# Kernel optimization log

Measured on AMD Instinct MI355X. Metric: run time of the kernel, lower is better.

## Reference

```python
import jax, jax.numpy as jnp
import numpy as np

B, N, H = 32, 1024, 128
EPS = 1e-5


def setup_inputs() -> dict:
    key = jax.random.key(0)
    ks = jax.random.split(key, 9)
    node_embeddings = jax.random.normal(ks[0], (B, N, H), dtype=jnp.float32)
    edge_relations = jax.random.normal(ks[1], (B, N, N, 3), dtype=jnp.float32)
    adjacency = jax.random.randint(ks[2], (N, N), 0, 2, dtype=jnp.int32)
    s_msg = 1.0 / np.sqrt(H + 3)
    s_upd = 1.0 / np.sqrt(2 * H)
    W_msg = jax.random.uniform(ks[3], (H, H + 3), jnp.float32, -s_msg, s_msg)
    b_msg = jax.random.uniform(ks[4], (H,), jnp.float32, -s_msg, s_msg)
    W_upd = jax.random.uniform(ks[5], (H, 2 * H), jnp.float32, -s_upd, s_upd)
    b_upd = jax.random.uniform(ks[6], (H,), jnp.float32, -s_upd, s_upd)
    gamma = jnp.ones((H,), jnp.float32)
    beta = jnp.zeros((H,), jnp.float32)
    return {"node_embeddings": node_embeddings, "edge_relations": edge_relations,
            "adjacency": adjacency, "W_msg": W_msg, "b_msg": b_msg,
            "W_upd": W_upd, "b_upd": b_upd, "gamma": gamma, "beta": beta}


def reference(node_embeddings, edge_relations, adjacency, W_msg, b_msg, W_upd, b_upd, gamma, beta):
    # node_embeddings: [B,N,H]; edge_relations: [B,N,N,3]; adjacency: [N,N]
    b_, n_, h_ = node_embeddings.shape
    mask = (adjacency > 0).astype(node_embeddings.dtype)  # mask[j,i]=1 if i is neighbor of j
    # Split msg_nn weight: Linear(cat(h_i, e_ij)) = h_i @ W_h^T + e_ij @ W_e^T + b
    W_h = W_msg[:, :h_]   # [H,H]
    W_e = W_msg[:, h_:]   # [H,3]
    h_part = jnp.einsum('bih,oh->bio', node_embeddings, W_h)       # [B,N,H]
    msg_h = jnp.einsum('ji,bio->bjo', mask, h_part)                # aggregate sender linear part
    e_agg = jnp.einsum('bijc,ji->bjc', edge_relations, mask)       # aggregate edge feats first (memory-bound)
    msg_e = jnp.einsum('bjc,oc->bjo', e_agg, W_e)
    deg = mask.sum(axis=1)                                         # [N] in-degree of j
    messages = msg_h + msg_e + deg[None, :, None] * b_msg          # bias added once per edge
    # Dropout(0.2) is identity in inference; BatchNorm uses batch stats (training-mode math).
    upd_in = jnp.concatenate([node_embeddings, messages], axis=-1)  # [B,N,2H]
    updated = jax.nn.relu(jnp.einsum('bjk,ok->bjo', upd_in, W_upd) + b_upd)
    flat = updated.reshape(-1, h_)
    mean = flat.mean(axis=0)
    var = flat.var(axis=0)  # biased, as BatchNorm1d
    normed = (flat - mean) * jax.lax.rsqrt(var + EPS) * gamma + beta
    return normed.reshape(b_, n_, h_) + node_embeddings
```

## Files before the change

kernel.cpp:

```cpp
#include <hip/hip_runtime.h>

typedef _Float16 f16;
typedef f16 f16x4 __attribute__((ext_vector_type(4)));
typedef f16 f16x8 __attribute__((ext_vector_type(8)));
typedef float f32x4 __attribute__((ext_vector_type(4)));

#define BB 32
#define NN 1024
#define HH 128
#define ROWS (BB*NN)
#define EPS 1e-5f

__device__ __forceinline__ f16 f2h(float x) { return (f16)x; }

typedef __attribute__((address_space(1))) const void gv_t;
typedef __attribute__((address_space(3))) void lv_t;
__device__ __forceinline__ void gl_lds16(const void* g, void* l) {
  __builtin_amdgcn_global_load_lds((gv_t*)g, (lv_t*)l, 16, 0, 0);
}

__global__ __launch_bounds__(256) void prep0_k(
    const float* __restrict__ W_msg, const float* __restrict__ W_upd,
    const float* __restrict__ node, const int* __restrict__ adj,
    f16* __restrict__ Wh, f16* __restrict__ Wupd, float* __restrict__ We,
    float* __restrict__ e_agg, float* __restrict__ deg, float* __restrict__ sums,
    f16* __restrict__ nodeh, f16* __restrict__ maskf, f16* __restrict__ maskT)
{
  const int blk = blockIdx.x, t = threadIdx.x;
  if (blk == 0) {
    for (int idx = t; idx < HH*HH; idx += 256) {
      const int o = idx >> 7, h = idx & 127;
      Wh[idx] = f2h(W_msg[o*131 + h]);
    }
  } else if (blk == 1) {
    for (int idx = t; idx < HH*256; idx += 256)
      Wupd[idx] = f2h(W_upd[idx]);
  } else if (blk == 2) {
    for (int idx = t; idx < HH*3; idx += 256)
      We[idx] = W_msg[(idx/3)*131 + 128 + (idx % 3)];
    if (t < 256) sums[t] = 0.f;
  } else if (blk < 7) {
    const int base = (blk - 3) * 24576 + t;
    #pragma unroll
    for (int r = 0; r < 96; r++) e_agg[base + r*256] = 0.f;
  } else if (blk < 15) {
    __shared__ f16 ldsT[128][136];
    __shared__ float degl[128];
    const int tj = blk - 7;
    if (t < 128) degl[t] = 0.f;
    __syncthreads();
    for (int ti = 0; ti < 8; ti++) {
      #pragma unroll
      for (int pass = 0; pass < 16; pass++) {
        const int q = pass*256 + t;
        const int row = q >> 5, c4 = (q & 31) << 2;
        const int4 m = *(const int4*)&adj[(long)(tj*128 + row)*NN + ti*128 + c4];
        f16x4 hv;
        hv[0] = (m.x > 0) ? (f16)1.0f : (f16)0.0f;
        hv[1] = (m.y > 0) ? (f16)1.0f : (f16)0.0f;
        hv[2] = (m.z > 0) ? (f16)1.0f : (f16)0.0f;
        hv[3] = (m.w > 0) ? (f16)1.0f : (f16)0.0f;
        *(f16x4*)&maskf[(long)(tj*128 + row)*NN + ti*128 + c4] = hv;
        ldsT[c4 + 0][row] = hv[0];
        ldsT[c4 + 1][row] = hv[1];
        ldsT[c4 + 2][row] = hv[2];
        ldsT[c4 + 3][row] = hv[3];
        const int cnt = (m.x > 0) + (m.y > 0) + (m.z > 0) + (m.w > 0);
        if (cnt) atomicAdd(&degl[row], (float)cnt);
      }
      __syncthreads();
      #pragma unroll
      for (int pass = 0; pass < 8; pass++) {
        const int q = pass*256 + t;
        const int rT = q >> 4, c8 = (q & 15) << 3;
        *(uint4*)&maskT[(long)(ti*128 + rT)*NN + tj*128 + c8] =
            *(const uint4*)&ldsT[rT][c8];
      }
      __syncthreads();
    }
    if (t < 128) deg[tj*128 + t] = degl[t];
  } else {
    const long base = (long)(blk - 15)*256 + t;
    #pragma unroll
    for (int p = 0; p < 64; p++) {
      const long idx = base + (long)p*16384;
      const float4 v = ((const float4*)node)[idx];
      f16x4 hv; hv[0] = f2h(v.x); hv[1] = f2h(v.y); hv[2] = f2h(v.z); hv[3] = f2h(v.w);
      *(f16x4*)&nodeh[idx << 2] = hv;
    }
  }
}

__global__ __launch_bounds__(256) void phaseB_k(
    const f16* __restrict__ nodeh, const float* __restrict__ E,
    const f16* __restrict__ maskT, const f16* __restrict__ Wh,
    f16* __restrict__ h_part_T, float* __restrict__ e_agg)
{
  __shared__ f16 As[128*32];
  __shared__ f16 Bs[128*32];
  const int tid = threadIdx.x;

  if (blockIdx.x >= 256) {
    const int e  = blockIdx.x - 256;
    const int bb = e >> 5;
    const int r5 = e & 31;
    const int jt = r5 & 3;
    const int ih = r5 >> 2;
    const int j  = (jt << 8) + tid;
    const int i0 = ih << 7;
    const float* Ep = E + (long)bb*3145728 + (long)i0*3072 + (long)j*3;
    const f16*   Mp = maskT + (long)i0*NN + j;
    float a0 = 0.f, a1 = 0.f, a2 = 0.f;
    for (int ii = 0; ii < 128; ii += 8) {
      float m[8];
      #pragma unroll
      for (int v = 0; v < 8; v++) m[v] = (float)Mp[(long)(ii + v)*NN];
      float ev[8][3];
      #pragma unroll
      for (int v = 0; v < 8; v++) {
        const float* q = Ep + (long)(ii + v)*3072;
        ev[v][0] = q[0]; ev[v][1] = q[1]; ev[v][2] = q[2];
      }
      #pragma unroll
      for (int v = 0; v < 8; v++) {
        a0 = fmaf(m[v], ev[v][0], a0);
        a1 = fmaf(m[v], ev[v][1], a1);
        a2 = fmaf(m[v], ev[v][2], a2);
      }
    }
    const long eb = ((long)bb*NN + j)*3;
    atomicAdd(&e_agg[eb],     a0);
    atomicAdd(&e_agg[eb + 1], a1);
    atomicAdd(&e_agg[eb + 2], a2);
    return;
  }

  const int g  = blockIdx.x;
  const int nt = g & 7, bb = g >> 3;
  const int nbase = nt << 7;
  const int lane = tid & 63, wave = tid >> 6;
  const int wm = (wave & 1) << 6, wn = (wave >> 1) << 6;

  f32x4 acc[2][4], acc2[2][4];
  #pragma unroll
  for (int i = 0; i < 2; i++)
    #pragma unroll
    for (int j = 0; j < 4; j++)
      #pragma unroll
      for (int r = 0; r < 4; r++) { acc[i][j][r] = 0.f; acc2[i][j][r] = 0.f; }

  for (int k0 = 0; k0 < HH; k0 += 32) {
    #pragma unroll
    for (int p = 0; p < 2; p++) {
      const int q = (p << 8) + tid;
      const int row = q >> 2, kp = (q & 3) << 3;
      gl_lds16(&Wh[(long)row*HH + k0 + kp], &As[q << 3]);
      gl_lds16(&nodeh[(long)((bb << 10) + nbase + row)*HH + k0 + kp], &Bs[q << 3]);
    }
    __syncthreads();
    f16x8 af[4], bf[4];
    #pragma unroll
    for (int i = 0; i < 4; i++) {
      af[i] = *(const f16x8*)&As[((wm + (i << 4) + (lane & 15)) << 5) + ((lane >> 4) << 3)];
      bf[i] = *(const f16x8*)&Bs[((wn + (i << 4) + (lane & 15)) << 5) + ((lane >> 4) << 3)];
    }
    #pragma unroll
    for (int i = 0; i < 2; i++)
      #pragma unroll
      for (int j = 0; j < 4; j++) {
        acc[i][j]  = __builtin_amdgcn_mfma_f32_16x16x32_f16(af[i],     bf[j], acc[i][j],  0, 0, 0);
        acc2[i][j] = __builtin_amdgcn_mfma_f32_16x16x32_f16(af[i + 2], bf[j], acc2[i][j], 0, 0, 0);
      }
    __syncthreads();
  }

  f16* out = h_part_T + (long)bb * (HH*NN);
  const int rb = (lane >> 4) << 2, cb = lane & 15;
  #pragma unroll
  for (int i = 0; i < 4; i++)
    #pragma unroll
    for (int r = 0; r < 4; r++) {
      const int gm = wm + (i << 4) + rb + r;
      #pragma unroll
      for (int j = 0; j < 4; j++) {
        const int gn = nbase + wn + (j << 4) + cb;
        const float v = (i < 2) ? acc[i][j][r] : acc2[i - 2][j][r];
        out[(long)gm*NN + gn] = f2h(v);
      }
    }
}

__global__ __launch_bounds__(256) void gemm1_k(
    const f16* __restrict__ maskf, const f16* __restrict__ hp,
    const float* __restrict__ deg, const float* __restrict__ b_msg,
    const float* __restrict__ e_agg, const float* __restrict__ We,
    f16* __restrict__ msgs)
{
  const int mt = blockIdx.x, bb = blockIdx.z;
  const int jb = mt << 7;
  __shared__ f16 As[128*32];
  __shared__ f16 Bs[128*32];
  const int tid = threadIdx.x, lane = tid & 63, wave = tid >> 6;
  const int wm = (wave & 1) << 6, wn = (wave >> 1) << 6;

  f32x4 acc[4][4];
  #pragma unroll
  for (int i = 0; i < 4; i++)
    #pragma unroll
    for (int j = 0; j < 4; j++)
      #pragma unroll
      for (int r = 0; r < 4; r++) acc[i][j][r] = 0.f;

  for (int k0 = 0; k0 < NN; k0 += 32) {
    #pragma unroll
    for (int p = 0; p < 2; p++) {
      const int q = (p << 8) + tid;
      const int row = q >> 2, kp = (q & 3) << 3;
      gl_lds16(&maskf[(long)(jb + row)*NN + k0 + kp], &As[q << 3]);
      gl_lds16(&hp[(long)bb*(HH*NN) + (long)row*NN + k0 + kp], &Bs[q << 3]);
    }
    __syncthreads();
    f16x8 af[4], bf[4];
    #pragma unroll
    for (int i = 0; i < 4; i++) {
      af[i] = *(const f16x8*)&As[((wm + (i << 4) + (lane & 15)) << 5) + ((lane >> 4) << 3)];
      bf[i] = *(const f16x8*)&Bs[((wn + (i << 4) + (lane & 15)) << 5) + ((lane >> 4) << 3)];
    }
    #pragma unroll
    for (int i = 0; i < 4; i++)
      #pragma unroll
      for (int j = 0; j < 4; j++)
        acc[i][j] = __builtin_amdgcn_mfma_f32_16x16x32_f16(af[i], bf[j], acc[i][j], 0, 0, 0);
    __syncthreads();
  }

  const int rb = (lane >> 4) << 2, cb = lane & 15;
  #pragma unroll
  for (int i = 0; i < 4; i++)
    #pragma unroll
    for (int r = 0; r < 4; r++) {
      const int gm = jb + wm + (i << 4) + rb + r;
      const float dg = deg[gm];
      const long eb = ((long)bb*NN + gm)*3;
      const float e0 = e_agg[eb], e1 = e_agg[eb+1], e2 = e_agg[eb+2];
      #pragma unroll
      for (int j = 0; j < 4; j++) {
        const int gn = wn + (j << 4) + cb;
        const float v = acc[i][j][r] + dg*b_msg[gn]
                      + e0*We[gn*3] + e1*We[gn*3+1] + e2*We[gn*3+2];
        msgs[((long)bb*NN + gm)*HH + gn] = f2h(v);
      }
    }
}

__global__ __launch_bounds__(256) void gemm2_k(
    const f16* __restrict__ nodeh, const f16* __restrict__ msgs,
    const f16* __restrict__ Wupd, const float* __restrict__ b_upd,
    f16* __restrict__ upd, float* __restrict__ sums)
{
  const int mt = blockIdx.x;
  const int rowb = mt << 7;
  __shared__ f16 As[128*32];
  __shared__ f16 Bs[128*32];
  __shared__ float colS[128], colQ[128];
  const int tid = threadIdx.x, lane = tid & 63, wave = tid >> 6;
  const int wm = (wave & 1) << 6, wn = (wave >> 1) << 6;
  if (tid < 128) { colS[tid] = 0.f; colQ[tid] = 0.f; }

  f32x4 acc[4][4];
  #pragma unroll
  for (int i = 0; i < 4; i++)
    #pragma unroll
    for (int j = 0; j < 4; j++)
      #pragma unroll
      for (int r = 0; r < 4; r++) acc[i][j][r] = 0.f;

  for (int k0 = 0; k0 < 256; k0 += 32) {
    #pragma unroll
    for (int p = 0; p < 2; p++) {
      const int q = (p << 8) + tid;
      const int row = q >> 2, kp = (q & 3) << 3;
      const f16* src = (k0 < HH)
        ? &nodeh[(long)(rowb + row)*HH + k0 + kp]
        : &msgs[(long)(rowb + row)*HH + (k0 - HH) + kp];
      gl_lds16(src, &As[q << 3]);
      gl_lds16(&Wupd[(long)row*256 + k0 + kp], &Bs[q << 3]);
    }
    __syncthreads();
    f16x8 af[4], bf[4];
    #pragma unroll
    for (int i = 0; i < 4; i++) {
      af[i] = *(const f16x8*)&As[((wm + (i << 4) + (lane & 15)) << 5) + ((lane >> 4) << 3)];
      bf[i] = *(const f16x8*)&Bs[((wn + (i << 4) + (lane & 15)) << 5) + ((lane >> 4) << 3)];
    }
    #pragma unroll
    for (int i = 0; i < 4; i++)
      #pragma unroll
      for (int j = 0; j < 4; j++)
        acc[i][j] = __builtin_amdgcn_mfma_f32_16x16x32_f16(af[i], bf[j], acc[i][j], 0, 0, 0);
    __syncthreads();
  }

  const int rb = (lane >> 4) << 2, cb = lane & 15;
  float bup[4], s[4] = {0,0,0,0}, qq[4] = {0,0,0,0};
  #pragma unroll
  for (int j = 0; j < 4; j++) bup[j] = b_upd[wn + (j << 4) + cb];
  #pragma unroll
  for (int i = 0; i < 4; i++)
    #pragma unroll
    for (int r = 0; r < 4; r++) {
      const int gm = rowb + wm + (i << 4) + rb + r;
      #pragma unroll
      for (int j = 0; j < 4; j++) {
        const int gn = wn + (j << 4) + cb;
        const float v = fmaxf(acc[i][j][r] + bup[j], 0.f);
        upd[(long)gm*HH + gn] = f2h(v);
        s[j] += v; qq[j] += v*v;
      }
    }
  #pragma unroll
  for (int j = 0; j < 4; j++) {
    const int gn = wn + (j << 4) + cb;
    atomicAdd(&colS[gn], s[j]);
    atomicAdd(&colQ[gn], qq[j]);
  }
  __syncthreads();
  if (tid < 128) {
    atomicAdd(&sums[tid],       colS[tid]);
    atomicAdd(&sums[128 + tid], colQ[tid]);
  }
}

__global__ __launch_bounds__(256) void final_k(const f16* __restrict__ upd,
    const float* __restrict__ node, const float* __restrict__ sums,
    const float* __restrict__ gamma, const float* __restrict__ beta,
    float* __restrict__ out)
{
  const long idx = (long)blockIdx.x*256 + threadIdx.x;
  const f16x4 u  = *(const f16x4*)&upd[idx << 2];
  const float4 nd = ((const float4*)node)[idx];
  const int ob = (idx & 31) << 2;
  const float inv = 1.0f/32768.0f;
  float4 res;
  #pragma unroll
  for (int c = 0; c < 4; c++) {
    const float m  = sums[ob + c]*inv;
    const float va = sums[128 + ob + c]*inv - m*m;
    const float sc = rsqrtf(va + EPS)*gamma[ob + c];
    ((float*)&res)[c] = ((float)u[c] - m)*sc + beta[ob + c]
                      + ((const float*)&nd)[c];
  }
  ((float4*)out)[idx] = res;
}

extern "C" void kernel_launch(void* const* d_in, const int* in_sizes, int n_in,
                              void* d_out, int out_size, void* d_ws, size_t ws_size,
                              hipStream_t stream) {
  const float* node  = (const float*)d_in[0];
  const float* E     = (const float*)d_in[1];
  const int*   adj   = (const int*)  d_in[2];
  const float* W_msg = (const float*)d_in[3];
  const float* b_msg = (const float*)d_in[4];
  const float* W_upd = (const float*)d_in[5];
  const float* b_upd = (const float*)d_in[6];
  const float* gamma = (const float*)d_in[7];
  const float* beta  = (const float*)d_in[8];
  float* out = (float*)d_out;

  char* p = (char*)d_ws;
  auto alloc = [&](size_t n) { void* r = (void*)p; p += (n + 255) & ~(size_t)255; return r; };
  f16*   h_part_T = (f16*)  alloc((size_t)BB*HH*NN*2);
  f16*   msgs     = (f16*)  alloc((size_t)ROWS*HH*2);
  f16*   upd      = (f16*)  alloc((size_t)ROWS*HH*2);
  f16*   nodeh    = (f16*)  alloc((size_t)ROWS*HH*2);
  f16*   maskf    = (f16*)  alloc((size_t)NN*NN*2);
  f16*   maskT    = (f16*)  alloc((size_t)NN*NN*2);
  float* e_agg    = (float*)alloc((size_t)BB*NN*3*4);
  f16*   Wh       = (f16*)  alloc((size_t)HH*HH*2);
  f16*   Wupd     = (f16*)  alloc((size_t)HH*256*2);
  float* We       = (float*)alloc((size_t)HH*3*4);
  float* deg      = (float*)alloc((size_t)NN*4);
  float* sums     = (float*)alloc((size_t)256*4);

  prep0_k<<<79, 256, 0, stream>>>(W_msg, W_upd, node, adj,
                                  Wh, Wupd, We, e_agg, deg, sums,
                                  nodeh, maskf, maskT);

  phaseB_k<<<1280, 256, 0, stream>>>(nodeh, E, maskT, Wh, h_part_T, e_agg);

  gemm1_k<<<dim3(8, 1, BB), 256, 0, stream>>>(maskf, h_part_T, deg, b_msg, e_agg, We, msgs);

  gemm2_k<<<256, 256, 0, stream>>>(nodeh, msgs, Wupd, b_upd, upd, sums);

  final_k<<<4096, 256, 0, stream>>>(upd, node, sums, gamma, beta, out);
}
```

Before: 690.5 us.

## Stage edge reads through LDS, fold degree bias into h_part, re-split prep work

The edge-aggregation blocks now copy contiguous 8-row chunks of edge_relations into LDS with global_load_lds, so global reads are coalesced instead of stride-3 per thread. The mask fragments are still read from global memory. The degree-times-bias term is folded into h_part as an added b_msg before the mask GEMM, which removes the deg computation and its LDS atomics. Prep work is spread over 131 blocks with one tile per transpose block, and the e_agg and sums zeroing moves to hipMemsetAsync. This adds extra launches and syncs in exchange for better memory coalescing and balance.

```diff
diff --git a/kernel.cpp b/kernel.cpp
--- a/kernel.cpp
+++ b/kernel.cpp
@@ -23,84 +23,70 @@
     const float* __restrict__ W_msg, const float* __restrict__ W_upd,
     const float* __restrict__ node, const int* __restrict__ adj,
     f16* __restrict__ Wh, f16* __restrict__ Wupd, float* __restrict__ We,
-    float* __restrict__ e_agg, float* __restrict__ deg, float* __restrict__ sums,
     f16* __restrict__ nodeh, f16* __restrict__ maskf, f16* __restrict__ maskT)
 {
   const int blk = blockIdx.x, t = threadIdx.x;
-  if (blk == 0) {
+  if (blk < 64) {
+    const long base = (long)blk*16384 + t;
+    #pragma unroll
+    for (int p = 0; p < 64; p++) {
+      const long idx = base + (long)p*256;
+      const float4 v = ((const float4*)node)[idx];
+      f16x4 hv; hv[0] = f2h(v.x); hv[1] = f2h(v.y); hv[2] = f2h(v.z); hv[3] = f2h(v.w);
+      *(f16x4*)&nodeh[idx << 2] = hv;
+    }
+  } else if (blk < 128) {
+    __shared__ f16 ldsT[128][136];
+    const int tt = blk - 64, tj = tt >> 3, ti = tt & 7;
+    #pragma unroll
+    for (int p = 0; p < 16; p++) {
+      const int q = p*256 + t;
+      const int row = q >> 5, c4 = (q & 31) << 2;
+      const int4 m = *(const int4*)&adj[(long)(tj*128 + row)*NN + ti*128 + c4];
+      f16x4 hv;
+      hv[0] = (m.x > 0) ? (f16)1.0f : (f16)0.0f;
+      hv[1] = (m.y > 0) ? (f16)1.0f : (f16)0.0f;
+      hv[2] = (m.z > 0) ? (f16)1.0f : (f16)0.0f;
+      hv[3] = (m.w > 0) ? (f16)1.0f : (f16)0.0f;
+      *(f16x4*)&maskf[(long)(tj*128 + row)*NN + ti*128 + c4] = hv;
+      ldsT[c4 + 0][row] = hv[0];
+      ldsT[c4 + 1][row] = hv[1];
+      ldsT[c4 + 2][row] = hv[2];
+      ldsT[c4 + 3][row] = hv[3];
+    }
+    __syncthreads();
+    #pragma unroll
+    for (int p = 0; p < 8; p++) {
+      const int q = p*256 + t;
+      const int rT = q >> 4, c8 = (q & 15) << 3;
+      *(uint4*)&maskT[(long)(ti*128 + rT)*NN + tj*128 + c8] =
+          *(const uint4*)&ldsT[rT][c8];
+    }
+  } else if (blk == 128) {
     for (int idx = t; idx < HH*HH; idx += 256) {
       const int o = idx >> 7, h = idx & 127;
       Wh[idx] = f2h(W_msg[o*131 + h]);
     }
-  } else if (blk == 1) {
+  } else if (blk == 129) {
     for (int idx = t; idx < HH*256; idx += 256)
       Wupd[idx] = f2h(W_upd[idx]);
-  } else if (blk == 2) {
+  } else {
     for (int idx = t; idx < HH*3; idx += 256)
       We[idx] = W_msg[(idx/3)*131 + 128 + (idx % 3)];
-    if (t < 256) sums[t] = 0.f;
-  } else if (blk < 7) {
-    const int base = (blk - 3) * 24576 + t;
-    #pragma unroll
-    for (int r = 0; r < 96; r++) e_agg[base + r*256] = 0.f;
-  } else if (blk < 15) {
-    __shared__ f16 ldsT[128][136];
-    __shared__ float degl[128];
-    const int tj = blk - 7;
-    if (t < 128) degl[t] = 0.f;
-    __syncthreads();
-    for (int ti = 0; ti < 8; ti++) {
-      #pragma unroll
-      for (int pass = 0; pass < 16; pass++) {
-        const int q = pass*256 + t;
-        const int row = q >> 5, c4 = (q & 31) << 2;
-        const int4 m = *(const int4*)&adj[(long)(tj*128 + row)*NN + ti*128 + c4];
-        f16x4 hv;
-        hv[0] = (m.x > 0) ? (f16)1.0f : (f16)0.0f;
-        hv[1] = (m.y > 0) ? (f16)1.0f : (f16)0.0f;
-        hv[2] = (m.z > 0) ? (f16)1.0f : (f16)0.0f;
-        hv[3] = (m.w > 0) ? (f16)1.0f : (f16)0.0f;
-        *(f16x4*)&maskf[(long)(tj*128 + row)*NN + ti*128 + c4] = hv;
-        ldsT[c4 + 0][row] = hv[0];
-        ldsT[c4 + 1][row] = hv[1];
-        ldsT[c4 + 2][row] = hv[2];
-        ldsT[c4 + 3][row] = hv[3];
-        const int cnt = (m.x > 0) + (m.y > 0) + (m.z > 0) + (m.w > 0);
-        if (cnt) atomicAdd(&degl[row], (float)cnt);
-      }
-      __syncthreads();
-      #pragma unroll
-      for (int pass = 0; pass < 8; pass++) {
-        const int q = pass*256 + t;
-        const int rT = q >> 4, c8 = (q & 15) << 3;
-        *(uint4*)&maskT[(long)(ti*128 + rT)*NN + tj*128 + c8] =
-            *(const uint4*)&ldsT[rT][c8];
-      }
-      __syncthreads();
-    }
-    if (t < 128) deg[tj*128 + t] = degl[t];
-  } else {
-    const long base = (long)(blk - 15)*256 + t;
-    #pragma unroll
-    for (int p = 0; p < 64; p++) {
-      const long idx = base + (long)p*16384;
-      const float4 v = ((const float4*)node)[idx];
-      f16x4 hv; hv[0] = f2h(v.x); hv[1] = f2h(v.y); hv[2] = f2h(v.z); hv[3] = f2h(v.w);
-      *(f16x4*)&nodeh[idx << 2] = hv;
-    }
   }
 }
 
 __global__ __launch_bounds__(256) void phaseB_k(
     const f16* __restrict__ nodeh, const float* __restrict__ E,
     const f16* __restrict__ maskT, const f16* __restrict__ Wh,
+    const float* __restrict__ b_msg,
     f16* __restrict__ h_part_T, float* __restrict__ e_agg)
 {
-  __shared__ f16 As[128*32];
-  __shared__ f16 Bs[128*32];
+  __shared__ __align__(16) char smem[24576];
   const int tid = threadIdx.x;
 
   if (blockIdx.x >= 256) {
+    float* Ebuf = (float*)smem;
     const int e  = blockIdx.x - 256;
     const int bb = e >> 5;
     const int r5 = e & 31;
@@ -108,24 +94,32 @@
     const int ih = r5 >> 2;
     const int j  = (jt << 8) + tid;
     const int i0 = ih << 7;
-    const float* Ep = E + (long)bb*3145728 + (long)i0*3072 + (long)j*3;
-    const f16*   Mp = maskT + (long)i0*NN + j;
+    const int lane = tid & 63, wv = tid >> 6;
+    const float* Eblk = E + (long)bb*3145728 + (long)i0*3072 + (long)(jt << 8)*3;
     float a0 = 0.f, a1 = 0.f, a2 = 0.f;
-    for (int ii = 0; ii < 128; ii += 8) {
-      float m[8];
-      #pragma unroll
-      for (int v = 0; v < 8; v++) m[v] = (float)Mp[(long)(ii + v)*NN];
-      float ev[8][3];
+    for (int ch = 0; ch < 16; ch++) {
+      const float* Ech = Eblk + (long)ch*8*3072;
+      __syncthreads();
+      #pragma unroll
+      for (int k = 0; k < 6; k++) {
+        const int m = wv*6 + k;
+        const int r = m/3;
+        const int cb = (m % 3) << 8;
+        gl_lds16(Ech + (long)r*3072 + cb + lane*4, Ebuf + m*256);
+      }
+      float mreg[8];
+      #pragma unroll
+      for (int v = 0; v < 8; v++)
+        mreg[v] = (float)maskT[(long)(i0 + ch*8 + v)*NN + j];
+      __syncthreads();
       #pragma unroll
       for (int v = 0; v < 8; v++) {
-        const float* q = Ep + (long)(ii + v)*3072;
-        ev[v][0] = q[0]; ev[v][1] = q[1]; ev[v][2] = q[2];
-      }
-      #pragma unroll
-      for (int v = 0; v < 8; v++) {
-        a0 = fmaf(m[v], ev[v][0], a0);
-        a1 = fmaf(m[v], ev[v][1], a1);
-        a2 = fmaf(m[v], ev[v][2], a2);
+        const float e0 = Ebuf[v*768 + tid*3];
+        const float e1 = Ebuf[v*768 + tid*3 + 1];
+        const float e2 = Ebuf[v*768 + tid*3 + 2];
+        a0 = fmaf(mreg[v], e0, a0);
+        a1 = fmaf(mreg[v], e1, a1);
+        a2 = fmaf(mreg[v], e2, a2);
       }
     }
     const long eb = ((long)bb*NN + j)*3;
@@ -135,6 +129,8 @@
     return;
   }
 
+  f16* As = (f16*)smem;
+  f16* Bs = (f16*)(smem + 8192);
   const int g  = blockIdx.x;
   const int nt = g & 7, bb = g >> 3;
   const int nbase = nt << 7;
@@ -181,10 +177,11 @@
     #pragma unroll
     for (int r = 0; r < 4; r++) {
       const int gm = wm + (i << 4) + rb + r;
+      const float bm = b_msg[gm];
       #pragma unroll
       for (int j = 0; j < 4; j++) {
         const int gn = nbase + wn + (j << 4) + cb;
-        const float v = (i < 2) ? acc[i][j][r] : acc2[i - 2][j][r];
+        const float v = ((i < 2) ? acc[i][j][r] : acc2[i - 2][j][r]) + bm;
         out[(long)gm*NN + gn] = f2h(v);
       }
     }
@@ -192,7 +189,6 @@
 
 __global__ __launch_bounds__(256) void gemm1_k(
     const f16* __restrict__ maskf, const f16* __restrict__ hp,
-    const float* __restrict__ deg, const float* __restrict__ b_msg,
     const float* __restrict__ e_agg, const float* __restrict__ We,
     f16* __restrict__ msgs)
 {
@@ -240,13 +236,12 @@
     #pragma unroll
     for (int r = 0; r < 4; r++) {
       const int gm = jb + wm + (i << 4) + rb + r;
-      const float dg = deg[gm];
       const long eb = ((long)bb*NN + gm)*3;
       const float e0 = e_agg[eb], e1 = e_agg[eb+1], e2 = e_agg[eb+2];
       #pragma unroll
       for (int j = 0; j < 4; j++) {
         const int gn = wn + (j << 4) + cb;
-        const float v = acc[i][j][r] + dg*b_msg[gn]
+        const float v = acc[i][j][r]
                       + e0*We[gn*3] + e1*We[gn*3+1] + e2*We[gn*3+2];
         msgs[((long)bb*NN + gm)*HH + gn] = f2h(v);
       }
@@ -379,16 +374,17 @@
   f16*   Wh       = (f16*)  alloc((size_t)HH*HH*2);
   f16*   Wupd     = (f16*)  alloc((size_t)HH*256*2);
   float* We       = (float*)alloc((size_t)HH*3*4);
-  float* deg      = (float*)alloc((size_t)NN*4);
   float* sums     = (float*)alloc((size_t)256*4);
 
-  prep0_k<<<79, 256, 0, stream>>>(W_msg, W_upd, node, adj,
-                                  Wh, Wupd, We, e_agg, deg, sums,
-                                  nodeh, maskf, maskT);
-
-  phaseB_k<<<1280, 256, 0, stream>>>(nodeh, E, maskT, Wh, h_part_T, e_agg);
-
-  gemm1_k<<<dim3(8, 1, BB), 256, 0, stream>>>(maskf, h_part_T, deg, b_msg, e_agg, We, msgs);
+  hipMemsetAsync(e_agg, 0, (size_t)BB*NN*3*4, stream);
+  hipMemsetAsync(sums,  0, (size_t)256*4, stream);
+
+  prep0_k<<<131, 256, 0, stream>>>(W_msg, W_upd, node, adj,
+                                   Wh, Wupd, We, nodeh, maskf, maskT);
+
+  phaseB_k<<<1280, 256, 0, stream>>>(nodeh, E, maskT, Wh, b_msg, h_part_T, e_agg);
+
+  gemm1_k<<<dim3(8, 1, BB), 256, 0, stream>>>(maskf, h_part_T, e_agg, We, msgs);
 
   gemm2_k<<<256, 256, 0, stream>>>(nodeh, msgs, Wupd, b_upd, upd, sums);
 
```

New measurement: 643.2 us. 6.9% less time.
